# Performance work log

Hardware: AMD Instinct MI355X
Metric: run time of the kernel (lower is better)

The kernel has to match this reference:

```python
import jax, jax.numpy as jnp
import numpy as np

B, S, E, H = 2, 2048, 2048, 16
D = E // H          # head_dim = 128
RD = 128            # rotary_emb_dim (== head_dim here)
BASE = 10000.0


def setup_inputs() -> dict:
    key = jax.random.key(0)
    k1, k2, k3, k4, k5 = jax.random.split(key, 5)
    scale = 0.02
    return {
        "x": jax.random.normal(k1, (B, S, E), dtype=jnp.float32),
        "wqkv_w": jax.random.normal(k2, (3 * E, E), dtype=jnp.float32) * scale,
        "wqkv_b": jax.random.normal(k3, (3 * E,), dtype=jnp.float32) * scale,
        "out_w": jax.random.normal(k4, (E, E), dtype=jnp.float32) * scale,
        "out_b": jax.random.normal(k5, (E,), dtype=jnp.float32) * scale,
    }


def _rope_cos_sin(seqlen, dtype):
    inv_freq = 1.0 / (BASE ** (jnp.arange(0, RD, 2, dtype=jnp.float32) / RD))
    t = jnp.arange(seqlen, dtype=jnp.float32)
    freqs = jnp.outer(t, inv_freq)          # (S, RD//2)
    return jnp.cos(freqs).astype(dtype), jnp.sin(freqs).astype(dtype)


def _apply_rotary(v, cos, sin):
    # v: (B, S, H, D); rotate first RD dims (here RD == D)
    v_rot, v_pass = v[..., :RD], v[..., RD:]
    v1, v2 = jnp.split(v_rot, 2, axis=-1)    # each (B, S, H, RD//2)
    c = cos[None, :, None, :]
    s = sin[None, :, None, :]
    rot = jnp.concatenate([v1 * c - v2 * s, v1 * s + v2 * c], axis=-1)
    return jnp.concatenate([rot, v_pass], axis=-1)


def reference(x, wqkv_w, wqkv_b, out_w, out_b):
    b, s, e = x.shape
    # column-parallel QKV projection (world size 1)
    qkv = jnp.einsum("bse,fe->bsf", x, wqkv_w) + wqkv_b     # (B, S, 3E)
    qkv = qkv.reshape(b, s, 3, H, D)
    cos, sin = _rope_cos_sin(s, x.dtype)
    q = _apply_rotary(qkv[:, :, 0], cos, sin)               # (B, S, H, D)
    k = _apply_rotary(qkv[:, :, 1], cos, sin)
    v = qkv[:, :, 2]
    # causal self-attention, softmax_scale = 1/sqrt(head_dim)
    scale = 1.0 / jnp.sqrt(jnp.asarray(D, dtype=x.dtype))
    scores = jnp.einsum("bshd,bthd->bhst", q, k) * scale    # (B, H, S, S)
    causal_mask = jnp.tril(jnp.ones((s, s), dtype=bool))
    scores = jnp.where(causal_mask[None, None], scores, jnp.finfo(x.dtype).min)
    probs = jax.nn.softmax(scores, axis=-1)
    ctx = jnp.einsum("bhst,bthd->bshd", probs, v)           # (B, S, H, D)
    # row-parallel output projection
    out = jnp.einsum("bse,fe->bsf", ctx.reshape(b, s, e), out_w) + out_b
    return out
```

## Files before the change

### kernel.cpp

```cpp
#include <hip/hip_runtime.h>
#include <cstdint>
#include <cstddef>

#define Bd 2
#define Sd 2048
#define Ed 2048
#define Hd 16
#define Dd 128
#define N3E 6144
#define ATT_SCALE 0.08838834764831845f
#define C2LOG 0.12751743f

typedef short bf16x8 __attribute__((ext_vector_type(8)));
typedef float f32x4 __attribute__((ext_vector_type(4)));
typedef float f32x16 __attribute__((ext_vector_type(16)));

__device__ __forceinline__ float bf2f(unsigned short u) {
    union { unsigned int u; float f; } c;
    c.u = ((unsigned int)u) << 16;
    return c.f;
}
__device__ __forceinline__ unsigned short f2bf(float f) {
    union { float f; unsigned int u; } c;
    c.f = f;
    unsigned int x = c.u;
    x += 0x7FFFu + ((x >> 16) & 1u);
    return (unsigned short)(x >> 16);
}

__device__ __forceinline__ float exp2_fast(float x) {
    float r;
    asm("v_exp_f32 %0, %1" : "=v"(r) : "v"(x));
    return r;
}
__device__ __forceinline__ unsigned int cvtpk_bf16(float lo, float hi) {
    unsigned int r;
    asm("v_cvt_pk_bf16_f32 %0, %1, %2" : "=v"(r) : "v"(lo), "v"(hi));
    return r;
}

__device__ __forceinline__ void gl2lds16(const void* g, void* l) {
    __builtin_amdgcn_global_load_lds(
        (const __attribute__((address_space(1))) void*)g,
        (__attribute__((address_space(3))) void*)l, 16, 0, 0);
}

__global__ void cvt_all(const float* __restrict__ x,
                        const float* __restrict__ w1,
                        const float* __restrict__ w2,
                        unsigned short* __restrict__ ox,
                        unsigned short* __restrict__ o1,
                        unsigned short* __restrict__ o2) {
    int i = (blockIdx.x * 256 + threadIdx.x) * 4;
    const float* s;
    unsigned short* d;
    int off;
    if (i < 8388608) { s = x; d = ox; off = i; }
    else if (i < 20971520) { s = w1; d = o1; off = i - 8388608; }
    else { s = w2; d = o2; off = i - 20971520; }
    const float4 v = *(const float4*)(s + off);
    d[off + 0] = f2bf(v.x);
    d[off + 1] = f2bf(v.y);
    d[off + 2] = f2bf(v.z);
    d[off + 3] = f2bf(v.w);
}

template <int MODE>
__global__ void gemm_bt(const unsigned short* __restrict__ A,
                        const unsigned short* __restrict__ Bm,
                        const float* __restrict__ bias,
                        void* __restrict__ o0, void* __restrict__ o1,
                        void* __restrict__ o2, int Ndim, int K) {
    __shared__ __align__(16) unsigned short U[16640];
    unsigned short* As = U;
    unsigned short* Bs = U + 8192;

    const int tid = threadIdx.x;
    const int lane = tid & 63;
    const int wave = tid >> 6;
    const int quad = lane >> 4;
    const int l16 = lane & 15;
    const int wr = wave >> 1;
    const int wc = wave & 1;

    const int n0 = blockIdx.x * 128;
    const int m0 = blockIdx.y * 128;

    const unsigned short* Ab = A + (size_t)m0 * K;
    const unsigned short* Bb = Bm + (size_t)n0 * K;

    const f32x4 fzero = {0.f, 0.f, 0.f, 0.f};
    f32x4 acc[4][4];
#pragma unroll
    for (int i = 0; i < 4; i++)
#pragma unroll
        for (int j = 0; j < 4; j++) acc[i][j] = fzero;

    for (int k0 = 0; k0 < K; k0 += 64) {
        __syncthreads();
#pragma unroll
        for (int it = 0; it < 4; ++it) {
            int L = it * 256 + tid;
            int row = L >> 3;
            int cs = L & 7;
            int gc = cs ^ (row & 7);
            gl2lds16(Ab + row * K + k0 + gc * 8, (void*)(As + L * 8));
            gl2lds16(Bb + row * K + k0 + gc * 8, (void*)(Bs + L * 8));
        }
        __syncthreads();
#pragma unroll
        for (int kk = 0; kk < 2; ++kk) {
            bf16x8 af[4], bfr[4];
#pragma unroll
            for (int i = 0; i < 4; i++) {
                int row = wr * 64 + i * 16 + l16;
                int cs = kk * 4 + quad;
                af[i] = *(const bf16x8*)(As + row * 64 + (cs ^ (row & 7)) * 8);
            }
#pragma unroll
            for (int j = 0; j < 4; j++) {
                int row = wc * 64 + j * 16 + l16;
                int cs = kk * 4 + quad;
                bfr[j] = *(const bf16x8*)(Bs + row * 64 + (cs ^ (row & 7)) * 8);
            }
#pragma unroll
            for (int i = 0; i < 4; i++)
#pragma unroll
                for (int j = 0; j < 4; j++)
                    acc[i][j] = __builtin_amdgcn_mfma_f32_16x16x32_bf16(
                        af[i], bfr[j], acc[i][j], 0, 0, 0);
        }
    }

    if (MODE == 0) {
#pragma unroll
        for (int j = 0; j < 4; j++) {
            int col = n0 + wc * 64 + j * 16 + l16;
            float bv = bias[col];
#pragma unroll
            for (int i = 0; i < 4; i++) {
                int rbase = m0 + wr * 64 + i * 16 + quad * 4;
#pragma unroll
                for (int r = 0; r < 4; r++)
                    ((float*)o0)[(size_t)(rbase + r) * Ndim + col] =
                        acc[i][j][r] + bv;
            }
        }
    } else {
        __syncthreads();
#pragma unroll
        for (int j = 0; j < 4; j++) {
            int coll = wc * 64 + j * 16 + l16;
            float bv = bias[n0 + coll];
#pragma unroll
            for (int i = 0; i < 4; i++) {
                int rl = wr * 64 + i * 16 + quad * 4;
#pragma unroll
                for (int r = 0; r < 4; r++)
                    U[(rl + r) * 130 + coll] = f2bf(acc[i][j][r] + bv);
            }
        }
        __syncthreads();

        const int ch = n0 >> 7;
        const int c = ch >> 4;
        const int h = ch & 15;
        const int bb = m0 >> 11;
        const int s0 = m0 & 2047;

        if (c < 2) {
            unsigned short* dstq = (unsigned short*)(c == 0 ? o0 : o1);
            const size_t hb = ((size_t)(bb * Hd + h)) * Sd;
#pragma unroll
            for (int it = 0; it < 16; ++it) {
                int lin = it * 256 + tid;
                int row = lin >> 5, p = lin & 31;
                int s = s0 + row;
                unsigned int lo = *(const unsigned int*)(U + row * 130 + 2 * p);
                unsigned int hi =
                    *(const unsigned int*)(U + row * 130 + 64 + 2 * p);
                float v1a = bf2f((unsigned short)lo), v1b = bf2f(lo >> 16);
                float v2a = bf2f((unsigned short)hi), v2b = bf2f(hi >> 16);
                float fa = (float)s * __expf(-(float)(2 * p) *
                                             (9.210340371976184f / 64.0f));
                float fb = (float)s * __expf(-(float)(2 * p + 1) *
                                             (9.210340371976184f / 64.0f));
                float sna, csa, snb, csb;
                __sincosf(fa, &sna, &csa);
                __sincosf(fb, &snb, &csb);
                ushort2 r1, r2;
                r1.x = f2bf(v1a * csa - v2a * sna);
                r1.y = f2bf(v1b * csb - v2b * snb);
                r2.x = f2bf(v1a * sna + v2a * csa);
                r2.y = f2bf(v1b * snb + v2b * csb);
                unsigned short* dst = dstq + (hb + s) * Dd;
                *(ushort2*)(dst + 2 * p) = r1;
                *(ushort2*)(dst + 64 + 2 * p) = r2;
            }
        } else {
            unsigned short* dstv = (unsigned short*)o2;
            const size_t hb = ((size_t)(bb * Hd + h)) * Dd;
#pragma unroll
            for (int it = 0; it < 16; ++it) {
                int lin = it * 256 + tid;
                int d = lin >> 5, sc = lin & 31;
                int s4 = sc * 4;
                ushort4 pk;
                pk.x = U[(s4 + 0) * 130 + d];
                pk.y = U[(s4 + 1) * 130 + d];
                pk.z = U[(s4 + 2) * 130 + d];
                pk.w = U[(s4 + 3) * 130 + d];
                *(ushort4*)(dstv + (hb + d) * Sd + s0 + s4) = pk;
            }
        }
    }
}

__global__ __launch_bounds__(256, 2) void flash_attn(
    const unsigned short* __restrict__ q, const unsigned short* __restrict__ k,
    const unsigned short* __restrict__ vt, unsigned short* __restrict__ ctx) {
    __shared__ __align__(16) unsigned short Ks[2][64 * 128];
    __shared__ __align__(16) unsigned short Vts[2][128 * 64];
    __shared__ __align__(16) unsigned short Ps[128 * 64];

    const int tid = threadIdx.x;
    const int lane = tid & 63;
    const int wave = tid >> 6;
    const int l32 = lane & 31;
    const int half = lane >> 5;

    const int yy = blockIdx.y;
    const int qi = (yy < 8) ? 15 - yy : yy - 8;
    const int bh = blockIdx.x;
    const int q0 = qi * 128;
    const int qg = q0 + wave * 32 + l32;
    const int prow = wave * 32 + l32;
    const int psw = prow & 7;

    const unsigned short* kb = k + (size_t)bh * Sd * Dd;
    const unsigned short* vtb = vt + (size_t)bh * Dd * Sd;

    bf16x8 aq[8];
    {
        const unsigned short* qrow = q + ((size_t)bh * Sd + qg) * Dd;
#pragma unroll
        for (int ks = 0; ks < 8; ks++)
            aq[ks] = *(const bf16x8*)(qrow + ks * 16 + half * 8);
    }

    f32x16 o[4];
#pragma unroll
    for (int db = 0; db < 4; db++)
#pragma unroll
        for (int r = 0; r < 16; r++) o[db][r] = 0.f;
    float mi = -3.0e38f, li = 0.f;

    auto stage = [&](int b, int t0) {
#pragma unroll
        for (int it = 0; it < 4; ++it) {
            int L = it * 256 + tid;
            int rk = L >> 4;
            int ck = L & 15;
            int gk = ck ^ (rk & 15);
            gl2lds16(kb + (size_t)(t0 + rk) * Dd + gk * 8,
                     (void*)(&Ks[b][0] + L * 8));
            int rv = L >> 3;
            int cv = L & 7;
            int gv = cv ^ (rv & 7);
            gl2lds16(vtb + (size_t)rv * Sd + t0 + gv * 8,
                     (void*)(&Vts[b][0] + L * 8));
        }
    };

    const int tmax = q0 + 64;
    stage(0, 0);
    int cur = 0;
    for (int t0 = 0; t0 <= tmax; t0 += 64) {
        __syncthreads();
        if (t0 + 64 <= tmax) stage(cur ^ 1, t0 + 64);

        if (t0 <= q0 + wave * 32 + 31) {
            const unsigned short* Ksc = &Ks[cur][0];
            const unsigned short* Vtsc = &Vts[cur][0];

            f32x16 sa[2];
#pragma unroll
            for (int b2 = 0; b2 < 2; b2++)
#pragma unroll
                for (int r = 0; r < 16; r++) sa[b2][r] = 0.f;
#pragma unroll
            for (int ks = 0; ks < 8; ks++) {
                int cd = ks * 2 + half;
#pragma unroll
                for (int b2 = 0; b2 < 2; b2++) {
                    int row = b2 * 32 + l32;
                    bf16x8 ak = *(const bf16x8*)(Ksc + row * 128 +
                                                 (cd ^ (row & 15)) * 8);
                    sa[b2] = __builtin_amdgcn_mfma_f32_32x32x16_bf16(
                        ak, aq[ks], sa[b2], 0, 0, 0);
                }
            }

            float mx = -3.0e38f;
            if (t0 + 63 > q0 + wave * 32) {
#pragma unroll
                for (int b2 = 0; b2 < 2; b2++)
#pragma unroll
                    for (int r = 0; r < 16; r++) {
                        float v = sa[b2][r] * C2LOG;
                        int tg = t0 + b2 * 32 + (r & 3) + 8 * (r >> 2) + 4 * half;
                        if (tg > qg) v = -3.0e38f;
                        sa[b2][r] = v;
                        mx = fmaxf(mx, v);
                    }
            } else {
#pragma unroll
                for (int b2 = 0; b2 < 2; b2++)
#pragma unroll
                    for (int r = 0; r < 16; r++) {
                        float v = sa[b2][r] * C2LOG;
                        sa[b2][r] = v;
                        mx = fmaxf(mx, v);
                    }
            }
            mx = fmaxf(mx, __shfl_xor(mx, 32, 64));

            if (mx > mi + 11.0f) {
                const float al = exp2_fast(mi - mx);
                mi = mx;
                li *= al;
#pragma unroll
                for (int db = 0; db < 4; db++)
#pragma unroll
                    for (int r = 0; r < 16; r++) o[db][r] *= al;
            }

            float rs = 0.f;
#pragma unroll
            for (int b2 = 0; b2 < 2; b2++)
#pragma unroll
                for (int g = 0; g < 4; g++) {
                    float p0 = exp2_fast(sa[b2][g * 4 + 0] - mi);
                    float p1 = exp2_fast(sa[b2][g * 4 + 1] - mi);
                    float p2 = exp2_fast(sa[b2][g * 4 + 2] - mi);
                    float p3 = exp2_fast(sa[b2][g * 4 + 3] - mi);
                    rs += (p0 + p1) + (p2 + p3);
                    uint2 w;
                    w.x = cvtpk_bf16(p0, p1);
                    w.y = cvtpk_bf16(p2, p3);
                    *(uint2*)(Ps + prow * 64 + ((b2 * 4 + g) ^ psw) * 8 +
                              half * 4) = w;
                }
            rs += __shfl_xor(rs, 32, 64);
            li += rs;

#pragma unroll
            for (int kk = 0; kk < 4; kk++) {
                bf16x8 bp = *(const bf16x8*)(Ps + prow * 64 +
                                             ((kk * 2 + half) ^ psw) * 8);
#pragma unroll
                for (int db = 0; db < 4; db++) {
                    int row = db * 32 + l32;
                    bf16x8 av = *(const bf16x8*)(
                        Vtsc + row * 64 + ((kk * 2 + half) ^ (row & 7)) * 8);
                    o[db] = __builtin_amdgcn_mfma_f32_32x32x16_bf16(
                        av, bp, o[db], 0, 0, 0);
                }
            }
        }
        cur ^= 1;
    }

    const int b = bh >> 4;
    const int h = bh & 15;
    const float inv = 1.0f / li;
    unsigned short* dst = ctx + ((size_t)(b * Sd + qg)) * Ed + h * Dd;
#pragma unroll
    for (int db = 0; db < 4; db++)
#pragma unroll
        for (int g = 0; g < 4; g++) {
            uint2 w;
            w.x = cvtpk_bf16(o[db][g * 4 + 0] * inv, o[db][g * 4 + 1] * inv);
            w.y = cvtpk_bf16(o[db][g * 4 + 2] * inv, o[db][g * 4 + 3] * inv);
            *(uint2*)(dst + db * 32 + g * 8 + half * 4) = w;
        }
}

extern "C" void kernel_launch(void* const* d_in, const int* in_sizes, int n_in,
                              void* d_out, int out_size, void* d_ws,
                              size_t ws_size, hipStream_t stream) {
    const float* x = (const float*)d_in[0];
    const float* wqkv_w = (const float*)d_in[1];
    const float* wqkv_b = (const float*)d_in[2];
    const float* out_w = (const float*)d_in[3];
    const float* out_b = (const float*)d_in[4];
    float* out = (float*)d_out;

    char* ws = (char*)d_ws;
    unsigned short* xb    = (unsigned short*)(ws + 0);
    unsigned short* wqkvb = (unsigned short*)(ws + 16777216);
    unsigned short* owb   = (unsigned short*)(ws + 41943040);
    unsigned short* qb    = (unsigned short*)(ws + 50331648);
    unsigned short* kb    = (unsigned short*)(ws + 67108864);
    unsigned short* vtb   = (unsigned short*)(ws + 83886080);
    unsigned short* ctx   = (unsigned short*)(ws + 0);

    cvt_all<<<24576, 256, 0, stream>>>(x, wqkv_w, out_w, xb, wqkvb, owb);
    gemm_bt<1><<<dim3(48, 32), 256, 0, stream>>>(xb, wqkvb, wqkv_b, qb, kb, vtb,
                                                 N3E, Ed);
    flash_attn<<<dim3(32, 16), 256, 0, stream>>>(qb, kb, vtb, ctx);
    gemm_bt<0><<<dim3(16, 32), 256, 0, stream>>>(ctx, owb, out_b, out, nullptr,
                                                 nullptr, Ed, Ed);
}
```

Measured before the change: 345.5 us.

## Single-buffer attention K/V tiles for higher occupancy; vectorize fp32-to-bf16 conversion

The flash attention kernel drops the double-buffered K/V LDS staging in favour of a single buffer and raises launch bounds to three blocks per CU. Fewer bytes of LDS per block should fit more blocks per CU, but the load of the next tile no longer overlaps with compute and each iteration now needs two barriers. Separately, the conversion kernel now handles eight elements per thread and writes them with packed bf16 conversion in one 16-byte store, using half as many blocks.

```diff
diff --git a/kernel.cpp b/kernel.cpp
--- a/kernel.cpp
+++ b/kernel.cpp
@@ -51,18 +51,21 @@
                         unsigned short* __restrict__ ox,
                         unsigned short* __restrict__ o1,
                         unsigned short* __restrict__ o2) {
-    int i = (blockIdx.x * 256 + threadIdx.x) * 4;
+    int i = (blockIdx.x * 256 + threadIdx.x) * 8;
     const float* s;
     unsigned short* d;
     int off;
     if (i < 8388608) { s = x; d = ox; off = i; }
     else if (i < 20971520) { s = w1; d = o1; off = i - 8388608; }
     else { s = w2; d = o2; off = i - 20971520; }
-    const float4 v = *(const float4*)(s + off);
-    d[off + 0] = f2bf(v.x);
-    d[off + 1] = f2bf(v.y);
-    d[off + 2] = f2bf(v.z);
-    d[off + 3] = f2bf(v.w);
+    const float4 v0 = *(const float4*)(s + off);
+    const float4 v1 = *(const float4*)(s + off + 4);
+    uint4 w;
+    w.x = cvtpk_bf16(v0.x, v0.y);
+    w.y = cvtpk_bf16(v0.z, v0.w);
+    w.z = cvtpk_bf16(v1.x, v1.y);
+    w.w = cvtpk_bf16(v1.z, v1.w);
+    *(uint4*)(d + off) = w;
 }
 
 template <int MODE>
@@ -216,11 +219,11 @@
     }
 }
 
-__global__ __launch_bounds__(256, 2) void flash_attn(
+__global__ __launch_bounds__(256, 3) void flash_attn(
     const unsigned short* __restrict__ q, const unsigned short* __restrict__ k,
     const unsigned short* __restrict__ vt, unsigned short* __restrict__ ctx) {
-    __shared__ __align__(16) unsigned short Ks[2][64 * 128];
-    __shared__ __align__(16) unsigned short Vts[2][128 * 64];
+    __shared__ __align__(16) unsigned short Ks[64 * 128];
+    __shared__ __align__(16) unsigned short Vts[128 * 64];
     __shared__ __align__(16) unsigned short Ps[128 * 64];
 
     const int tid = threadIdx.x;
@@ -255,34 +258,28 @@
         for (int r = 0; r < 16; r++) o[db][r] = 0.f;
     float mi = -3.0e38f, li = 0.f;
 
-    auto stage = [&](int b, int t0) {
+    auto stage = [&](int t0) {
 #pragma unroll
         for (int it = 0; it < 4; ++it) {
             int L = it * 256 + tid;
             int rk = L >> 4;
             int ck = L & 15;
             int gk = ck ^ (rk & 15);
-            gl2lds16(kb + (size_t)(t0 + rk) * Dd + gk * 8,
-                     (void*)(&Ks[b][0] + L * 8));
+            gl2lds16(kb + (size_t)(t0 + rk) * Dd + gk * 8, (void*)(Ks + L * 8));
             int rv = L >> 3;
             int cv = L & 7;
             int gv = cv ^ (rv & 7);
-            gl2lds16(vtb + (size_t)rv * Sd + t0 + gv * 8,
-                     (void*)(&Vts[b][0] + L * 8));
+            gl2lds16(vtb + (size_t)rv * Sd + t0 + gv * 8, (void*)(Vts + L * 8));
         }
     };
 
     const int tmax = q0 + 64;
-    stage(0, 0);
-    int cur = 0;
     for (int t0 = 0; t0 <= tmax; t0 += 64) {
+        if (t0) __syncthreads();
+        stage(t0);
         __syncthreads();
-        if (t0 + 64 <= tmax) stage(cur ^ 1, t0 + 64);
 
         if (t0 <= q0 + wave * 32 + 31) {
-            const unsigned short* Ksc = &Ks[cur][0];
-            const unsigned short* Vtsc = &Vts[cur][0];
-
             f32x16 sa[2];
 #pragma unroll
             for (int b2 = 0; b2 < 2; b2++)
@@ -294,7 +291,7 @@
 #pragma unroll
                 for (int b2 = 0; b2 < 2; b2++) {
                     int row = b2 * 32 + l32;
-                    bf16x8 ak = *(const bf16x8*)(Ksc + row * 128 +
+                    bf16x8 ak = *(const bf16x8*)(Ks + row * 128 +
                                                  (cd ^ (row & 15)) * 8);
                     sa[b2] = __builtin_amdgcn_mfma_f32_32x32x16_bf16(
                         ak, aq[ks], sa[b2], 0, 0, 0);
@@ -362,13 +359,12 @@
                 for (int db = 0; db < 4; db++) {
                     int row = db * 32 + l32;
                     bf16x8 av = *(const bf16x8*)(
-                        Vtsc + row * 64 + ((kk * 2 + half) ^ (row & 7)) * 8);
+                        Vts + row * 64 + ((kk * 2 + half) ^ (row & 7)) * 8);
                     o[db] = __builtin_amdgcn_mfma_f32_32x32x16_bf16(
                         av, bp, o[db], 0, 0, 0);
                 }
             }
         }
-        cur ^= 1;
     }
 
     const int b = bh >> 4;
@@ -405,7 +401,7 @@
     unsigned short* vtb   = (unsigned short*)(ws + 83886080);
     unsigned short* ctx   = (unsigned short*)(ws + 0);
 
-    cvt_all<<<24576, 256, 0, stream>>>(x, wqkv_w, out_w, xb, wqkvb, owb);
+    cvt_all<<<12288, 256, 0, stream>>>(x, wqkv_w, out_w, xb, wqkvb, owb);
     gemm_bt<1><<<dim3(48, 32), 256, 0, stream>>>(xb, wqkvb, wqkv_b, qb, kb, vtb,
                                                  N3E, Ed);
     flash_attn<<<dim3(32, 16), 256, 0, stream>>>(qb, kb, vtb, ctx);
```

Measured after the change: 427.6 us. +23.8%, slower.

## Keep softmax probabilities in registers via permlane swap, widen conversion kernel

Applied to the files above, without the earlier changes.

The attention kernel no longer stages the bf16 probability tile through shared memory. It packs the probabilities in registers and uses v_permlane32_swap to rearrange them into the B-operand layout for the PV MFMA, which removes an LDS write/read round trip and frees LDS. The fp32-to-bf16 conversion kernel now handles 8 elements per thread with packed conversion and a single 16-byte store, launching half as many blocks. The query-tile-to-block mapping is also reordered, which changes how the causal work is balanced across blocks.

```diff
diff --git a/kernel.cpp b/kernel.cpp
--- a/kernel.cpp
+++ b/kernel.cpp
@@ -51,18 +51,21 @@
                         unsigned short* __restrict__ ox,
                         unsigned short* __restrict__ o1,
                         unsigned short* __restrict__ o2) {
-    int i = (blockIdx.x * 256 + threadIdx.x) * 4;
+    int i = (blockIdx.x * 256 + threadIdx.x) * 8;
     const float* s;
     unsigned short* d;
     int off;
     if (i < 8388608) { s = x; d = ox; off = i; }
     else if (i < 20971520) { s = w1; d = o1; off = i - 8388608; }
     else { s = w2; d = o2; off = i - 20971520; }
-    const float4 v = *(const float4*)(s + off);
-    d[off + 0] = f2bf(v.x);
-    d[off + 1] = f2bf(v.y);
-    d[off + 2] = f2bf(v.z);
-    d[off + 3] = f2bf(v.w);
+    const float4 v0 = *(const float4*)(s + off);
+    const float4 v1 = *(const float4*)(s + off + 4);
+    uint4 w;
+    w.x = cvtpk_bf16(v0.x, v0.y);
+    w.y = cvtpk_bf16(v0.z, v0.w);
+    w.z = cvtpk_bf16(v1.x, v1.y);
+    w.w = cvtpk_bf16(v1.z, v1.w);
+    *(uint4*)(d + off) = w;
 }
 
 template <int MODE>
@@ -221,7 +224,6 @@
     const unsigned short* __restrict__ vt, unsigned short* __restrict__ ctx) {
     __shared__ __align__(16) unsigned short Ks[2][64 * 128];
     __shared__ __align__(16) unsigned short Vts[2][128 * 64];
-    __shared__ __align__(16) unsigned short Ps[128 * 64];
 
     const int tid = threadIdx.x;
     const int lane = tid & 63;
@@ -229,13 +231,11 @@
     const int l32 = lane & 31;
     const int half = lane >> 5;
 
-    const int yy = blockIdx.y;
-    const int qi = (yy < 8) ? 15 - yy : yy - 8;
     const int bh = blockIdx.x;
+    const int y = blockIdx.y;
+    const int qi = ((y & 7) << 1) + (y >> 3);
     const int q0 = qi * 128;
     const int qg = q0 + wave * 32 + l32;
-    const int prow = wave * 32 + l32;
-    const int psw = prow & 7;
 
     const unsigned short* kb = k + (size_t)bh * Sd * Dd;
     const unsigned short* vtb = vt + (size_t)bh * Dd * Sd;
@@ -339,32 +339,48 @@
 #pragma unroll
             for (int b2 = 0; b2 < 2; b2++)
 #pragma unroll
-                for (int g = 0; g < 4; g++) {
-                    float p0 = exp2_fast(sa[b2][g * 4 + 0] - mi);
-                    float p1 = exp2_fast(sa[b2][g * 4 + 1] - mi);
-                    float p2 = exp2_fast(sa[b2][g * 4 + 2] - mi);
-                    float p3 = exp2_fast(sa[b2][g * 4 + 3] - mi);
-                    rs += (p0 + p1) + (p2 + p3);
-                    uint2 w;
-                    w.x = cvtpk_bf16(p0, p1);
-                    w.y = cvtpk_bf16(p2, p3);
-                    *(uint2*)(Ps + prow * 64 + ((b2 * 4 + g) ^ psw) * 8 +
-                              half * 4) = w;
+                for (int r = 0; r < 16; r++) {
+                    float pp = exp2_fast(sa[b2][r] - mi);
+                    sa[b2][r] = pp;
+                    rs += pp;
                 }
             rs += __shfl_xor(rs, 32, 64);
             li += rs;
 
+            bf16x8 bp[4];
+#pragma unroll
+            for (int b2 = 0; b2 < 2; b2++) {
+                unsigned int w0 = cvtpk_bf16(sa[b2][0], sa[b2][1]);
+                unsigned int w1 = cvtpk_bf16(sa[b2][2], sa[b2][3]);
+                unsigned int w2 = cvtpk_bf16(sa[b2][4], sa[b2][5]);
+                unsigned int w3 = cvtpk_bf16(sa[b2][6], sa[b2][7]);
+                unsigned int w4 = cvtpk_bf16(sa[b2][8], sa[b2][9]);
+                unsigned int w5 = cvtpk_bf16(sa[b2][10], sa[b2][11]);
+                unsigned int w6 = cvtpk_bf16(sa[b2][12], sa[b2][13]);
+                unsigned int w7 = cvtpk_bf16(sa[b2][14], sa[b2][15]);
+                asm volatile("v_permlane32_swap_b32 %0, %1"
+                             : "+v"(w0), "+v"(w2));
+                asm volatile("v_permlane32_swap_b32 %0, %1"
+                             : "+v"(w1), "+v"(w3));
+                asm volatile("v_permlane32_swap_b32 %0, %1"
+                             : "+v"(w4), "+v"(w6));
+                asm volatile("v_permlane32_swap_b32 %0, %1"
+                             : "+v"(w5), "+v"(w7));
+                uint4 u0 = {w0, w1, w2, w3};
+                uint4 u1 = {w4, w5, w6, w7};
+                bp[2 * b2] = *reinterpret_cast<bf16x8*>(&u0);
+                bp[2 * b2 + 1] = *reinterpret_cast<bf16x8*>(&u1);
+            }
+
 #pragma unroll
             for (int kk = 0; kk < 4; kk++) {
-                bf16x8 bp = *(const bf16x8*)(Ps + prow * 64 +
-                                             ((kk * 2 + half) ^ psw) * 8);
 #pragma unroll
                 for (int db = 0; db < 4; db++) {
                     int row = db * 32 + l32;
                     bf16x8 av = *(const bf16x8*)(
                         Vtsc + row * 64 + ((kk * 2 + half) ^ (row & 7)) * 8);
                     o[db] = __builtin_amdgcn_mfma_f32_32x32x16_bf16(
-                        av, bp, o[db], 0, 0, 0);
+                        av, bp[kk], o[db], 0, 0, 0);
                 }
             }
         }
@@ -405,7 +421,7 @@
     unsigned short* vtb   = (unsigned short*)(ws + 83886080);
     unsigned short* ctx   = (unsigned short*)(ws + 0);
 
-    cvt_all<<<24576, 256, 0, stream>>>(x, wqkv_w, out_w, xb, wqkvb, owb);
+    cvt_all<<<12288, 256, 0, stream>>>(x, wqkv_w, out_w, xb, wqkvb, owb);
     gemm_bt<1><<<dim3(48, 32), 256, 0, stream>>>(xb, wqkvb, wqkv_b, qb, kb, vtb,
                                                  N3E, Ed);
     flash_attn<<<dim3(32, 16), 256, 0, stream>>>(qb, kb, vtb, ctx);
```

Result: slower. 360.4 us (+4.3%).
